# Optimization experiments

Hardware: AMD Instinct MI355X
Metric: run time of the kernel (lower is better)

The kernel has to match this reference:

```python
import jax, jax.numpy as jnp
import numpy as np

N_NODES = 100000
N_EDGES = 1600000
F_IN = 512
D_EMB = 128
D_HID = 64
N_CLS = 32
EPS = 1e-5


def setup_inputs() -> dict:
    key = jax.random.key(0)
    ks = jax.random.split(key, 16)
    def w(k, shape):
        fan_in = shape[0]
        return jax.random.normal(k, shape, dtype=jnp.float32) / jnp.sqrt(jnp.float32(fan_in))
    return {
        "x": jax.random.normal(ks[0], (N_NODES, F_IN), dtype=jnp.float32),
        "W1": w(ks[1], (F_IN, D_EMB)), "b1": jnp.zeros((D_EMB,), jnp.float32),
        "Wc1": w(ks[2], (D_EMB, D_HID)), "bc1": jnp.zeros((D_HID,), jnp.float32),
        "Wc2": w(ks[3], (D_HID, D_HID)), "bc2": jnp.zeros((D_HID,), jnp.float32),
        "Wc3": w(ks[4], (D_HID, D_HID)), "bc3": jnp.zeros((D_HID,), jnp.float32),
        "gamma": jnp.ones((D_HID,), jnp.float32), "beta": jnp.zeros((D_HID,), jnp.float32),
        "W2": w(ks[5], (D_HID, N_CLS)), "b2": jnp.zeros((N_CLS,), jnp.float32),
        "W3": w(ks[6], (N_CLS, N_CLS)), "b3": jnp.zeros((N_CLS,), jnp.float32),
        "edge_index": jax.random.randint(ks[7], (2, N_EDGES), 0, N_NODES, dtype=jnp.int32),
    }


def _agg_mean(h, src, dst, n):
    # gather source-node features along edges, sum into destination nodes, divide by degree
    s = jax.ops.segment_sum(h[src], dst, num_segments=n)          # [N, d]
    deg = jax.ops.segment_sum(jnp.ones((src.shape[0], 1), h.dtype), dst, num_segments=n)
    return s / jnp.maximum(deg, 1.0)


def _conv1p(h, src, dst, W, b):
    # ConvolutionalLayer_1P: neighborhood gather/aggregate -> linear -> relu
    return jax.nn.relu(_agg_mean(h, src, dst, h.shape[0]) @ W + b)


def reference(x, W1, b1, Wc1, bc1, Wc2, bc2, Wc3, bc3, gamma, beta, W2, b2, W3, b3, edge_index):
    src, dst = edge_index[0], edge_index[1]
    # linmaps1 on 0th-order ptensors == identity copy
    h = jax.nn.relu(x @ W1 + b1)                 # lin1 + relu (dropout = identity in eval)
    h = _conv1p(h, src, dst, Wc1, bc1)           # conv1
    h = _conv1p(h, src, dst, Wc2, bc2)           # conv2
    h = _conv1p(h, src, dst, Wc3, bc3)           # conv3
    mean = jnp.mean(h, axis=0)
    var = jnp.var(h, axis=0)
    h = (h - mean) * jax.lax.rsqrt(var + EPS) * gamma + beta  # batchnorm (batch stats)
    h = jax.nn.relu(h @ W2 + b2)                 # lin2 + relu (dropout = identity)
    out = h @ W3 + b3                            # lin3; linmaps0 == identity
    return out
```

## Files before the change

### kernel.cpp

```cpp
#include <hip/hip_runtime.h>
#include <cstdint>
#include <cstddef>

constexpr int F_IN  = 512;
constexpr int D_EMB = 128;
constexpr int D_HID = 64;
constexpr int N_CLS = 32;

typedef __attribute__((ext_vector_type(8))) short short8;
typedef __attribute__((ext_vector_type(4))) float floatx4;

__device__ inline unsigned short f2bf(float f) {
  union { float f; uint32_t u; } v; v.f = f;
  uint32_t r = v.u + 0x7FFF + ((v.u >> 16) & 1);
  return (unsigned short)(r >> 16);
}

__global__ __launch_bounds__(256) void wt_kernel(
    const float* __restrict__ W1, short8* __restrict__ Wt2)
{
  int idx = blockIdx.x * 256 + threadIdx.x;
  int kc8 = idx >> 10, lin = idx & 1023;
  int ct = lin >> 7, rem = lin & 127, ks = rem >> 6, ln = rem & 63;
  int col = ct * 16 + (ln & 15);
  int k0 = kc8 * 64 + ks * 32 + (ln >> 4) * 8;
  short8 s;
#pragma unroll
  for (int j = 0; j < 8; ++j)
    s[j] = (short)f2bf(W1[(size_t)(k0 + j) * D_EMB + col]);
  Wt2[idx] = s;
}

__global__ __launch_bounds__(256) void lin1_mfma_kernel(
    const float* __restrict__ X, const short8* __restrict__ Wt2,
    const float* __restrict__ b1, float* __restrict__ H1, int n)
{
  __shared__ short8 Ws[1024];
  __shared__ short8 Xs[1024];

  const int t = threadIdx.x;
  const int wave = t >> 6, lane = t & 63;
  const int quad = lane >> 4, mrow = lane & 15;
  const int node0 = blockIdx.x * 128;
  const int rloc = (wave >> 1) * 64;
  const int cw = (wave & 1) * 4;

  const float* sp[4];
  int srow[4], soff[4];
#pragma unroll
  for (int i = 0; i < 4; ++i) {
    int g = t + i * 256;
    int row = g >> 3, col8 = g & 7;
    srow[i] = row;
    soff[i] = row * 128 + ((col8 * 16) ^ ((row & 7) << 4));
    int gr = node0 + row; if (gr >= n) gr = n - 1;
    sp[i] = &X[(size_t)gr * F_IN + col8 * 8];
  }

  floatx4 acc[4][4];
#pragma unroll
  for (int i = 0; i < 4; ++i)
#pragma unroll
    for (int j = 0; j < 4; ++j) acc[i][j] = (floatx4){0.f, 0.f, 0.f, 0.f};

  for (int kc8 = 0; kc8 < 8; ++kc8) {
    __syncthreads();
#pragma unroll
    for (int i = 0; i < 4; ++i) {
      int lin = t + i * 256;
      Ws[lin] = Wt2[kc8 * 1024 + lin];
    }
#pragma unroll
    for (int i = 0; i < 4; ++i) {
      const float* p = sp[i] + kc8 * 64;
      float4 v0 = *(const float4*)p;
      float4 v1 = *(const float4*)(p + 4);
      short8 s;
      s[0] = (short)f2bf(v0.x); s[1] = (short)f2bf(v0.y);
      s[2] = (short)f2bf(v0.z); s[3] = (short)f2bf(v0.w);
      s[4] = (short)f2bf(v1.x); s[5] = (short)f2bf(v1.y);
      s[6] = (short)f2bf(v1.z); s[7] = (short)f2bf(v1.w);
      *(short8*)((char*)Xs + soff[i]) = s;
    }
    __syncthreads();

#pragma unroll
    for (int ks = 0; ks < 2; ++ks) {
      short8 af[4], bf[4];
#pragma unroll
      for (int rt = 0; rt < 4; ++rt) {
        int row = rloc + rt * 16 + mrow;
        int byteoff = row * 128 + ((ks * 64 + quad * 16) ^ ((row & 7) << 4));
        af[rt] = *(const short8*)((const char*)Xs + byteoff);
      }
#pragma unroll
      for (int c = 0; c < 4; ++c)
        bf[c] = Ws[((cw + c) * 2 + ks) * 64 + lane];
#pragma unroll
      for (int rt = 0; rt < 4; ++rt)
#pragma unroll
        for (int c = 0; c < 4; ++c)
          acc[rt][c] = __builtin_amdgcn_mfma_f32_16x16x32_bf16(
              af[rt], bf[c], acc[rt][c], 0, 0, 0);
    }
  }

  const int rowbase = node0 + rloc;
#pragma unroll
  for (int ct = 0; ct < 4; ++ct) {
    int col = (cw + ct) * 16 + mrow;
    float bias = b1[col];
#pragma unroll
    for (int rt = 0; rt < 4; ++rt) {
#pragma unroll
      for (int r = 0; r < 4; ++r) {
        int gn = rowbase + rt * 16 + quad * 4 + r;
        if (gn < n)
          H1[(size_t)gn * D_EMB + col] = fmaxf(acc[rt][ct][r] + bias, 0.f);
      }
    }
  }
}

template<int K, bool PRE>
__global__ __launch_bounds__(256) void mm_kernel(
    const float* __restrict__ In, const int* __restrict__ deg,
    const float* __restrict__ bin, const float* __restrict__ W,
    float* __restrict__ Out, int n)
{
  __shared__ float Hs[64][K + 4];
  __shared__ float Ws[K][64];
  const int t = threadIdx.x;
  const int node0 = blockIdx.x * 64;
  constexpr int KQ = K / 4;

#pragma unroll
  for (int i = 0; i < (64 * KQ) / 256; ++i) {
    int lin = t + i * 256;
    int node = lin / KQ, kq = lin % KQ;
    int gn = node0 + node;
    float4 v = make_float4(0.f, 0.f, 0.f, 0.f);
    if (gn < n) {
      v = *(const float4*)&In[(size_t)gn * K + kq * 4];
      if (PRE) {
        float rd = 1.f / fmaxf((float)deg[gn], 1.f);
        v.x = fmaxf(v.x * rd + bin[kq * 4 + 0], 0.f);
        v.y = fmaxf(v.y * rd + bin[kq * 4 + 1], 0.f);
        v.z = fmaxf(v.z * rd + bin[kq * 4 + 2], 0.f);
        v.w = fmaxf(v.w * rd + bin[kq * 4 + 3], 0.f);
      }
    }
    *(float4*)&Hs[node][kq * 4] = v;
  }
#pragma unroll
  for (int i = 0; i < (K * 64) / 1024; ++i) {
    int lin = t + i * 256;
    ((float4*)&Ws[0][0])[lin] = ((const float4*)W)[lin];
  }
  __syncthreads();

  const int rg = t >> 4, cg = t & 15;
  float acc[4][4];
#pragma unroll
  for (int i = 0; i < 4; ++i)
#pragma unroll
    for (int j = 0; j < 4; ++j) acc[i][j] = 0.f;

#pragma unroll 8
  for (int k = 0; k < K; ++k) {
    float a[4] = {Hs[rg*4+0][k], Hs[rg*4+1][k], Hs[rg*4+2][k], Hs[rg*4+3][k]};
    float4 b = *(const float4*)&Ws[k][cg * 4];
#pragma unroll
    for (int i = 0; i < 4; ++i) {
      acc[i][0] += a[i]*b.x; acc[i][1] += a[i]*b.y;
      acc[i][2] += a[i]*b.z; acc[i][3] += a[i]*b.w;
    }
  }
#pragma unroll
  for (int i = 0; i < 4; ++i) {
    int gn = node0 + rg * 4 + i;
    if (gn < n) {
      float4 o = make_float4(acc[i][0], acc[i][1], acc[i][2], acc[i][3]);
      *(float4*)&Out[(size_t)gn * 64 + cg * 4] = o;
    }
  }
}


__global__ __launch_bounds__(256) void hist_kernel(
    const int* __restrict__ dst, int* __restrict__ G, int nE, int B, int NB)
{
  __shared__ int h[256];
  int blk = blockIdx.x, t = threadIdx.x;
  h[t] = 0;
  __syncthreads();
  int base = blk * 8192;
  int lim = min(8192, nE - base);
  for (int i = t; i < lim; i += 256)
    atomicAdd(&h[dst[base + i] >> 9], 1);
  __syncthreads();
  if (t < NB) G[t * B + blk] = h[t];
}

__global__ __launch_bounds__(256) void scan1_kernel(
    const int* __restrict__ in, int* __restrict__ out,
    int* __restrict__ bsum, int n)
{
  __shared__ int sh[256];
  int t = threadIdx.x;
  int i = blockIdx.x * 256 + t;
  int c = (i < n) ? in[i] : 0;
  sh[t] = c;
  __syncthreads();
#pragma unroll
  for (int off = 1; off < 256; off <<= 1) {
    int v = 0;
    if (t >= off) v = sh[t - off];
    __syncthreads();
    if (t >= off) sh[t] += v;
    __syncthreads();
  }
  if (i < n) out[i] = sh[t] - c;
  if (t == 255) bsum[blockIdx.x] = sh[255];
}

__global__ __launch_bounds__(256) void scan2_kernel(int* __restrict__ bsum, int nb)
{
  __shared__ int sh[256];
  __shared__ int carry;
  int t = threadIdx.x;
  if (t == 0) carry = 0;
  __syncthreads();
  for (int base = 0; base < nb; base += 256) {
    int i = base + t;
    int v = (i < nb) ? bsum[i] : 0;
    sh[t] = v;
    __syncthreads();
#pragma unroll
    for (int off = 1; off < 256; off <<= 1) {
      int u = 0;
      if (t >= off) u = sh[t - off];
      __syncthreads();
      if (t >= off) sh[t] += u;
      __syncthreads();
    }
    int c0 = carry;
    int incl = sh[t], total = sh[255];
    if (i < nb) bsum[i] = c0 + incl - v;
    __syncthreads();
    if (t == 0) carry = c0 + total;
    __syncthreads();
  }
  if (t == 0) bsum[nb] = carry;
}

__global__ __launch_bounds__(256) void scan3_kernel(
    int* __restrict__ W, const int* __restrict__ bsum, int NG, int nb)
{
  int i = blockIdx.x * 256 + threadIdx.x;
  if (i < NG) W[i] += bsum[i >> 8];
  else if (i == NG) W[NG] = bsum[nb];
}

__global__ __launch_bounds__(256) void scatter2_kernel(
    const int* __restrict__ src, const int* __restrict__ dst,
    const int* __restrict__ W, int2* __restrict__ EP, int nE, int B, int NB)
{
  __shared__ int cur[256];
  int blk = blockIdx.x, t = threadIdx.x;
  if (t < NB) cur[t] = W[t * B + blk];
  __syncthreads();
  int base = blk * 8192;
  int lim = min(8192, nE - base);
  for (int i = t; i < lim; i += 256) {
    int s = src[base + i], d = dst[base + i];
    int slot = atomicAdd(&cur[d >> 9], 1);
    EP[slot] = make_int2(s, d);
  }
}

__global__ __launch_bounds__(256) void fillc_kernel(
    const int2* __restrict__ EP, const int* __restrict__ W,
    int* __restrict__ cnt, int* __restrict__ offs, int* __restrict__ adj,
    int n, int nE, int B, int NB)
{
  __shared__ int h[512];
  int b = blockIdx.x, t = threadIdx.x;
  int segStart = W[b * B];
  int segEnd = (b == NB - 1) ? nE : W[(b + 1) * B];
  int nodeBase = b << 9;

  h[t] = 0; h[t + 256] = 0;
  __syncthreads();
  for (int i = segStart + t; i < segEnd; i += 256)
    atomicAdd(&h[EP[i].y - nodeBase], 1);
  __syncthreads();
  int c0 = h[t], c1 = h[t + 256];
#pragma unroll
  for (int off = 1; off < 512; off <<= 1) {
    int a = (t >= off) ? h[t - off] : 0;
    int bb = (t + 256 >= off) ? h[t + 256 - off] : 0;
    __syncthreads();
    h[t] += a; h[t + 256] += bb;
    __syncthreads();
  }
  int e0 = h[t] - c0, e1 = h[t + 256] - c1;
  int g0 = nodeBase + t, g1 = nodeBase + t + 256;
  if (g0 < n) { cnt[g0] = c0; offs[g0] = segStart + e0; }
  if (g1 < n) { cnt[g1] = c1; offs[g1] = segStart + e1; }
  if (b == 0 && t == 0) offs[n] = nE;
  __syncthreads();
  h[t] = e0; h[t + 256] = e1;
  __syncthreads();
  for (int i = segStart + t; i < segEnd; i += 256) {
    int2 p = EP[i];
    int slot = atomicAdd(&h[p.y - nodeBase], 1);
    adj[segStart + slot] = p.x;
  }
}

__global__ __launch_bounds__(256) void gather_kernel(
    const float* __restrict__ P, const int* __restrict__ offs,
    const int* __restrict__ adj, float* __restrict__ A, int n)
{
  int node = (blockIdx.x * 256 + threadIdx.x) >> 6;
  int lane = threadIdx.x & 63;
  if (node >= n) return;
  int beg = offs[node], end = offs[node + 1];
  float acc0 = 0.f, acc1 = 0.f;
  int j = beg;
  while (j < end) {
    int m = min(end - j, 64);
    int idx = (lane < m) ? adj[j + lane] : 0;
    int q = 0;
    for (; q + 1 < m; q += 2) {
      int s0 = __shfl(idx, q, 64);
      int s1 = __shfl(idx, q + 1, 64);
      acc0 += P[(size_t)s0 * 64 + lane];
      acc1 += P[(size_t)s1 * 64 + lane];
    }
    if (q < m) {
      int s0 = __shfl(idx, q, 64);
      acc0 += P[(size_t)s0 * 64 + lane];
    }
    j += m;
  }
  A[(size_t)node * 64 + lane] = acc0 + acc1;
}

__global__ __launch_bounds__(256) void post3_kernel(
    const float* __restrict__ A, const int* __restrict__ deg,
    const float* __restrict__ bc3, float* __restrict__ H4,
    float* __restrict__ stats, int n)
{
  int t = threadIdx.x;
  int f = t & 63, q = t >> 6;
  float b = bc3[f];
  float s = 0.f, s2 = 0.f;
  for (int node = blockIdx.x * 4 + q; node < n; node += gridDim.x * 4) {
    float v = fmaxf(A[(size_t)node * 64 + f] / fmaxf((float)deg[node], 1.f) + b, 0.f);
    H4[(size_t)node * 64 + f] = v;
    s += v; s2 += v * v;
  }
  __shared__ float red[2][4][64];
  red[0][q][f] = s; red[1][q][f] = s2;
  __syncthreads();
  if (t < 128) {
    int which = t >> 6, ff = t & 63;
    float a = red[which][0][ff] + red[which][1][ff] +
              red[which][2][ff] + red[which][3][ff];
    atomicAdd(&stats[which * 64 + ff], a);
  }
}

__global__ __launch_bounds__(256) void fold_kernel(
    const float* __restrict__ stats, const float* __restrict__ gamma,
    const float* __restrict__ beta, const float* __restrict__ W2,
    const float* __restrict__ b2, float* __restrict__ W2f,
    float* __restrict__ b2f, int n)
{
  __shared__ float rsg[64], corr[64];
  int t = threadIdx.x;
  if (t < 64) {
    float m = stats[t] / (float)n;
    float var = stats[64 + t] / (float)n - m * m;
    float rs = rsqrtf(var + 1e-5f);
    float g = gamma[t] * rs;
    rsg[t] = g;
    corr[t] = beta[t] - m * g;
  }
  __syncthreads();
#pragma unroll
  for (int i = 0; i < 8; ++i) {
    int lin = t + i * 256;
    int k = lin >> 5;
    W2f[lin] = rsg[k] * W2[lin];
  }
  if (t < 32) {
    float a = b2[t];
    for (int k = 0; k < 64; ++k) a += corr[k] * W2[k * 32 + t];
    b2f[t] = a;
  }
}

__global__ __launch_bounds__(256) void final_kernel(
    const float* __restrict__ H4, const float* __restrict__ W2f,
    const float* __restrict__ b2f, const float* __restrict__ W3,
    const float* __restrict__ b3, float* __restrict__ Out, int n)
{
  __shared__ float Hs[64][68];
  __shared__ float W2s[64][32];
  __shared__ float W3s[32][32];
  __shared__ float Us[64][36];
  __shared__ float b2s[32], b3s[32];
  const int t = threadIdx.x;
  const int node0 = blockIdx.x * 64;

#pragma unroll
  for (int i = 0; i < 4; ++i) {
    int lin = t + i * 256;
    int node = lin >> 4, kq = lin & 15;
    float4 v = make_float4(0.f, 0.f, 0.f, 0.f);
    if (node0 + node < n)
      v = *(const float4*)&H4[(size_t)(node0 + node) * 64 + kq * 4];
    *(float4*)&Hs[node][kq * 4] = v;
  }
#pragma unroll
  for (int i = 0; i < 2; ++i) {
    int lin = t + i * 256;
    ((float4*)&W2s[0][0])[lin] = ((const float4*)W2f)[lin];
  }
  ((float4*)&W3s[0][0])[t & 255] = ((const float4*)W3)[t & 255];
  if (t < 32) { b2s[t] = b2f[t]; b3s[t] = b3[t]; }
  __syncthreads();

  const int rg = t >> 4, cg = t & 15;
  float acc[4][2] = {{0.f,0.f},{0.f,0.f},{0.f,0.f},{0.f,0.f}};
#pragma unroll 8
  for (int k = 0; k < 64; ++k) {
    float a[4] = {Hs[rg*4+0][k], Hs[rg*4+1][k], Hs[rg*4+2][k], Hs[rg*4+3][k]};
    float w0 = W2s[k][cg*2], w1 = W2s[k][cg*2+1];
#pragma unroll
    for (int i = 0; i < 4; ++i) { acc[i][0] += a[i]*w0; acc[i][1] += a[i]*w1; }
  }
#pragma unroll
  for (int i = 0; i < 4; ++i) {
    Us[rg*4+i][cg*2+0] = fmaxf(acc[i][0] + b2s[cg*2+0], 0.f);
    Us[rg*4+i][cg*2+1] = fmaxf(acc[i][1] + b2s[cg*2+1], 0.f);
  }
  __syncthreads();

  float acc2[4][2] = {{0.f,0.f},{0.f,0.f},{0.f,0.f},{0.f,0.f}};
#pragma unroll
  for (int k = 0; k < 32; ++k) {
    float a[4] = {Us[rg*4+0][k], Us[rg*4+1][k], Us[rg*4+2][k], Us[rg*4+3][k]};
    float w0 = W3s[k][cg*2], w1 = W3s[k][cg*2+1];
#pragma unroll
    for (int i = 0; i < 4; ++i) { acc2[i][0] += a[i]*w0; acc2[i][1] += a[i]*w1; }
  }
  float (*Os)[36] = (float(*)[36])Hs;
#pragma unroll
  for (int i = 0; i < 4; ++i) {
    Os[rg*4+i][cg*2+0] = acc2[i][0] + b3s[cg*2+0];
    Os[rg*4+i][cg*2+1] = acc2[i][1] + b3s[cg*2+1];
  }
  __syncthreads();
#pragma unroll
  for (int i = 0; i < 2; ++i) {
    int lin = t + i * 256;
    int node = lin >> 3, c4 = lin & 7;
    if (node0 + node < n)
      *(float4*)&Out[(size_t)(node0 + node) * 32 + c4 * 4] =
          *(float4*)&Os[node][c4 * 4];
  }
}

extern "C" void kernel_launch(void* const* d_in, const int* in_sizes, int n_in,
                              void* d_out, int out_size, void* d_ws, size_t ws_size,
                              hipStream_t stream)
{
  const float* X     = (const float*)d_in[0];
  const float* W1    = (const float*)d_in[1];
  const float* b1    = (const float*)d_in[2];
  const float* Wc1   = (const float*)d_in[3];
  const float* bc1   = (const float*)d_in[4];
  const float* Wc2   = (const float*)d_in[5];
  const float* bc2   = (const float*)d_in[6];
  const float* Wc3   = (const float*)d_in[7];
  const float* bc3   = (const float*)d_in[8];
  const float* gamma = (const float*)d_in[9];
  const float* beta  = (const float*)d_in[10];
  const float* W2    = (const float*)d_in[11];
  const float* b2    = (const float*)d_in[12];
  const float* W3    = (const float*)d_in[13];
  const float* b3    = (const float*)d_in[14];
  const int*   ei    = (const int*)d_in[15];

  const int n  = in_sizes[0] / F_IN;
  const int nE = in_sizes[15] / 2;
  const int* src  = ei;
  const int* dstv = ei + nE;

  const int NB = (n + 511) >> 9;
  const int B  = (nE + 8191) >> 13;
  const int NG = NB * B;
  const int nbG = (NG + 255) / 256;

  float* ws    = (float*)d_ws;
  float* H1    = ws;
  float* P     = H1 + (size_t)n * D_EMB;
  float* A     = P  + (size_t)n * D_HID;
  float* stats = A  + (size_t)n * D_HID;
  float* W2f   = stats + 128;
  float* b2f   = W2f + 2048;
  int*   cnt   = (int*)(b2f + 32);
  int*   offs  = cnt + n;
  int*   G     = offs + n + 1;
  int*   W     = G + NG;
  int*   bsum  = W + NG + 1;
  int*   adj   = bsum + nbG + 1;
  uintptr_t epAddr = ((uintptr_t)(adj + nE) + 7) & ~(uintptr_t)7;
  int2*  EP    = (int2*)epAddr;
  short8* Wt2  = (short8*)(EP + nE);
  float* H4    = H1;

  const int nb  = (n + 63) / 64;
  const int gatherBlocks = (int)(((long long)n * 64 + 255) / 256);

  hipMemsetAsync(stats, 0, 128 * sizeof(float), stream);

  wt_kernel<<<32, 256, 0, stream>>>(W1, Wt2);
  lin1_mfma_kernel<<<(n + 127) / 128, 256, 0, stream>>>(X, Wt2, b1, H1, n);

  hist_kernel<<<B, 256, 0, stream>>>(dstv, G, nE, B, NB);
  scan1_kernel<<<nbG, 256, 0, stream>>>(G, W, bsum, NG);
  scan2_kernel<<<1, 256, 0, stream>>>(bsum, nbG);
  scan3_kernel<<<(NG + 256) / 256, 256, 0, stream>>>(W, bsum, NG, nbG);
  scatter2_kernel<<<B, 256, 0, stream>>>(src, dstv, W, EP, nE, B, NB);
  fillc_kernel<<<NB, 256, 0, stream>>>(EP, W, cnt, offs, adj, n, nE, B, NB);

  mm_kernel<128, false><<<nb, 256, 0, stream>>>(H1, nullptr, nullptr, Wc1, P, n);
  gather_kernel<<<gatherBlocks, 256, 0, stream>>>(P, offs, adj, A, n);

  mm_kernel<64, true><<<nb, 256, 0, stream>>>(A, cnt, bc1, Wc2, P, n);
  gather_kernel<<<gatherBlocks, 256, 0, stream>>>(P, offs, adj, A, n);

  mm_kernel<64, true><<<nb, 256, 0, stream>>>(A, cnt, bc2, Wc3, P, n);
  gather_kernel<<<gatherBlocks, 256, 0, stream>>>(P, offs, adj, A, n);

  post3_kernel<<<256, 256, 0, stream>>>(A, cnt, bc3, H4, stats, n);

  fold_kernel<<<1, 256, 0, stream>>>(stats, gamma, beta, W2, b2, W2f, b2f, n);
  final_kernel<<<nb, 256, 0, stream>>>(H4, W2f, b2f, W3, b3, (float*)d_out, n);
}
```

Measured before the change: 728.8 us.

## Prefetch next K-chunk of X and W into registers during MFMA compute in lin1

```diff
diff --git a/kernel.cpp b/kernel.cpp
--- a/kernel.cpp
+++ b/kernel.cpp
@@ -46,12 +46,11 @@
   const int cw = (wave & 1) * 4;
 
   const float* sp[4];
-  int srow[4], soff[4];
+  int soff[4];
 #pragma unroll
   for (int i = 0; i < 4; ++i) {
     int g = t + i * 256;
     int row = g >> 3, col8 = g & 7;
-    srow[i] = row;
     soff[i] = row * 128 + ((col8 * 16) ^ ((row & 7) << 4));
     int gr = node0 + row; if (gr >= n) gr = n - 1;
     sp[i] = &X[(size_t)gr * F_IN + col8 * 8];
@@ -63,26 +62,43 @@
 #pragma unroll
     for (int j = 0; j < 4; ++j) acc[i][j] = (floatx4){0.f, 0.f, 0.f, 0.f};
 
+  float4 xr[4][2];
+  short8 wr[4];
+
+#pragma unroll
+  for (int i = 0; i < 4; ++i) {
+    const float* p = sp[i];
+    xr[i][0] = *(const float4*)p;
+    xr[i][1] = *(const float4*)(p + 4);
+    wr[i] = Wt2[t + i * 256];
+  }
+
   for (int kc8 = 0; kc8 < 8; ++kc8) {
-    __syncthreads();
+    short8 s8[4];
 #pragma unroll
     for (int i = 0; i < 4; ++i) {
-      int lin = t + i * 256;
-      Ws[lin] = Wt2[kc8 * 1024 + lin];
-    }
+      s8[i][0] = (short)f2bf(xr[i][0].x); s8[i][1] = (short)f2bf(xr[i][0].y);
+      s8[i][2] = (short)f2bf(xr[i][0].z); s8[i][3] = (short)f2bf(xr[i][0].w);
+      s8[i][4] = (short)f2bf(xr[i][1].x); s8[i][5] = (short)f2bf(xr[i][1].y);
+      s8[i][6] = (short)f2bf(xr[i][1].z); s8[i][7] = (short)f2bf(xr[i][1].w);
+    }
+    __syncthreads();
 #pragma unroll
     for (int i = 0; i < 4; ++i) {
-      const float* p = sp[i] + kc8 * 64;
-      float4 v0 = *(const float4*)p;
-      float4 v1 = *(const float4*)(p + 4);
-      short8 s;
-      s[0] = (short)f2bf(v0.x); s[1] = (short)f2bf(v0.y);
-      s[2] = (short)f2bf(v0.z); s[3] = (short)f2bf(v0.w);
-      s[4] = (short)f2bf(v1.x); s[5] = (short)f2bf(v1.y);
-      s[6] = (short)f2bf(v1.z); s[7] = (short)f2bf(v1.w);
-      *(short8*)((char*)Xs + soff[i]) = s;
-    }
-    __syncthreads();
+      *(short8*)((char*)Xs + soff[i]) = s8[i];
+      Ws[t + i * 256] = wr[i];
+    }
+    __syncthreads();
+
+    if (kc8 < 7) {
+#pragma unroll
+      for (int i = 0; i < 4; ++i) {
+        const float* p = sp[i] + (kc8 + 1) * 64;
+        xr[i][0] = *(const float4*)p;
+        xr[i][1] = *(const float4*)(p + 4);
+        wr[i] = Wt2[(kc8 + 1) * 1024 + t + i * 256];
+      }
+    }
 
 #pragma unroll
     for (int ks = 0; ks < 2; ++ks) {
```

New measurement: 730.1 us. No clear change (+0.2%).
